# Optimization experiments

Hardware: AMD Instinct MI355X
Metric: run time of the kernel (lower is better)

Reference implementation:

```python
import jax, jax.numpy as jnp
import numpy as np

N_NODES = 100000   # n_nodes
N_EDGES = 1600000  # n_nodes * avg_degree(16)
D_IN = 128
D_OUT = 128


def setup_inputs() -> dict:
    key = jax.random.key(0)
    k1, k2, k3, k4, k5 = jax.random.split(key, 5)
    h = jax.random.normal(k1, (N_NODES, D_IN), dtype=jnp.float32)
    edge_src = jax.random.randint(k2, (N_EDGES,), 0, N_NODES, dtype=jnp.int32)
    edge_dst = jax.random.randint(k3, (N_EDGES,), 0, N_NODES, dtype=jnp.int32)
    # Linear params, init per reset_parameters: U(-stdv, stdv), stdv = 1/sqrt(in_feats)
    stdv = 1.0 / np.sqrt(D_IN)
    W = jax.random.uniform(k4, (D_OUT, D_IN), dtype=jnp.float32, minval=-stdv, maxval=stdv)
    b = jax.random.uniform(k5, (D_OUT,), dtype=jnp.float32, minval=-stdv, maxval=stdv)
    return {"h": h, "edge_src": edge_src, "edge_dst": edge_dst, "W": W, "b": b}


def reference(h, edge_src, edge_dst, W, b):
    # update_all(copy_src('h'), sum) == neighbor-sum aggregation (SpMM with 0/1 adjacency)
    ah = jax.ops.segment_sum(h[edge_src], edge_dst, num_segments=N_NODES)  # [N, D_IN]
    # dense linear + activation fused on the aggregated features
    return jax.nn.relu(ah @ W.T + b)  # [N, D_OUT]
```

## Files before the change

kernel.cpp:

```cpp
#include <hip/hip_runtime.h>

#define D 128
#define BKT_SHIFT 9
#define BKT_SIZE 512
#define P1_EPB 4096
#define CNT_EPB 8192
#define SW_LDU 68

typedef __attribute__((ext_vector_type(8))) short bf16x8;
typedef __attribute__((ext_vector_type(4))) float f32x4;

__device__ inline unsigned int pack2bf(float a, float b) {
    unsigned int ua = __float_as_uint(a);
    unsigned int ub = __float_as_uint(b);
    ua = (ua + 0x7fffu + ((ua >> 16) & 1u)) >> 16;
    ub = (ub + 0x7fffu + ((ub >> 16) & 1u)) >> 16;
    return ua | (ub << 16);
}
__device__ inline unsigned short pack1bf(float a) {
    unsigned int ua = __float_as_uint(a);
    return (unsigned short)((ua + 0x7fffu + ((ua >> 16) & 1u)) >> 16);
}


__global__ __launch_bounds__(256) void bucket_count_kernel(
    const int* __restrict__ edst, int* __restrict__ bucketCnt, int n_edges, int nbk)
{
    __shared__ int hcnt[256];
    const int tid = threadIdx.x;
    hcnt[tid] = 0;
    __syncthreads();
    const int base = blockIdx.x * CNT_EPB;
    const int lim = min(CNT_EPB, n_edges - base);
    for (int k = tid; k < lim; k += 256)
        atomicAdd(&hcnt[edst[base + k] >> BKT_SHIFT], 1);
    __syncthreads();
    if (tid < nbk && hcnt[tid] > 0) atomicAdd(&bucketCnt[tid], hcnt[tid]);
}

__global__ __launch_bounds__(256) void bucket_scan_kernel(
    const int* __restrict__ bucketCnt, int* __restrict__ bucketBase,
    int* __restrict__ bucketCur, int nbk)
{
    __shared__ int s[256];
    const int t = threadIdx.x;
    int v = (t < nbk) ? bucketCnt[t] : 0;
    s[t] = v;
    __syncthreads();
    #pragma unroll
    for (int off = 1; off < 256; off <<= 1) {
        int x = (t >= off) ? s[t - off] : 0;
        __syncthreads();
        s[t] += x;
        __syncthreads();
    }
    if (t < nbk) {
        int base = s[t] - v;
        bucketBase[t] = base;
        bucketCur[t] = base;
    }
}

__global__ __launch_bounds__(256) void p1_partition_kernel(
    const int* __restrict__ esrc, const int* __restrict__ edst,
    int* __restrict__ bucketCur, unsigned int* __restrict__ pairs, int n_edges)
{
    __shared__ int hcnt[256];
    __shared__ int hbase[256];
    const int tid = threadIdx.x;
    const int base = blockIdx.x * P1_EPB;
    hcnt[tid] = 0;
    __syncthreads();
    unsigned int pk[16]; int bk[16];
    #pragma unroll
    for (int k = 0; k < 16; k++) {
        int e = base + k * 256 + tid;
        if (e < n_edges) {
            int sv = esrc[e], dv = edst[e];
            bk[k] = dv >> BKT_SHIFT;
            pk[k] = ((unsigned)sv << BKT_SHIFT) | (unsigned)(dv & (BKT_SIZE - 1));
            atomicAdd(&hcnt[bk[k]], 1);
        } else bk[k] = -1;
    }
    __syncthreads();
    int cval = hcnt[tid];
    if (cval > 0) hbase[tid] = atomicAdd(&bucketCur[tid], cval);
    hcnt[tid] = 0;
    __syncthreads();
    #pragma unroll
    for (int k = 0; k < 16; k++) {
        if (bk[k] >= 0) {
            int loc = atomicAdd(&hcnt[bk[k]], 1);
            pairs[hbase[bk[k]] + loc] = pk[k];
        }
    }
}

__global__ __launch_bounds__(256) void p2_sort_kernel(
    const unsigned int* __restrict__ pairs, const int* __restrict__ bucketBase,
    int* __restrict__ sorted_src, int* __restrict__ gstart, int* __restrict__ gend,
    int n_nodes, int n_edges, int nbk)
{
    __shared__ int hist[BKT_SIZE];
    __shared__ int cur[BKT_SIZE];
    __shared__ int sb[256];
    const int tid = threadIdx.x;
    const int bkt = blockIdx.x;
    const int nbase = bkt << BKT_SHIFT;
    const int pstart = bucketBase[bkt];
    const int pend = (bkt == nbk - 1) ? n_edges : bucketBase[bkt + 1];
    hist[tid] = 0; hist[tid + 256] = 0;
    __syncthreads();
    for (int j = pstart + tid; j < pend; j += 256)
        atomicAdd(&hist[pairs[j] & (BKT_SIZE - 1)], 1);
    __syncthreads();
    int a  = hist[2 * tid];
    int b2 = hist[2 * tid + 1];
    int psum = a + b2;
    sb[tid] = psum;
    __syncthreads();
    #pragma unroll
    for (int off = 1; off < 256; off <<= 1) {
        int x = (tid >= off) ? sb[tid - off] : 0;
        __syncthreads();
        sb[tid] += x;
        __syncthreads();
    }
    int pexcl = sb[tid] - psum;
    cur[2 * tid] = pexcl;
    cur[2 * tid + 1] = pexcl + a;
    __syncthreads();
    for (int i = tid; i < BKT_SIZE; i += 256) {
        int nd = nbase + i;
        if (nd < n_nodes) {
            int st = pstart + cur[i];
            gstart[nd] = st;
            gend[nd] = st + hist[i];
        }
    }
    __syncthreads();
    for (int j = pstart + tid; j < pend; j += 256) {
        unsigned int p = pairs[j];
        int local = p & (BKT_SIZE - 1);
        int pos = pstart + atomicAdd(&cur[local], 1);
        sorted_src[pos] = (int)(p >> BKT_SHIFT);
    }
}

__global__ __launch_bounds__(256) void gemm_z_kernel(
    const float* __restrict__ h, const float* __restrict__ W,
    unsigned short* __restrict__ z, int n_nodes)
{
    __shared__ unsigned int sW[128 * SW_LDU];
    const int tid = threadIdx.x;
    for (int i = tid; i < 4096; i += 256) {
        float4 w = ((const float4*)W)[i];
        int row = i >> 5, c4 = i & 31;
        unsigned int* dst = &sW[row * SW_LDU + c4 * 2];
        dst[0] = pack2bf(w.x, w.y);
        dst[1] = pack2bf(w.z, w.w);
    }
    __syncthreads();

    const int wave = tid >> 6;
    const int lane = tid & 63;
    const int m = lane & 15;
    const int q = lane >> 4;
    const int r0 = blockIdx.x * 64 + wave * 16;
    const int arow = r0 + m;
    const bool rvalid = arow < n_nodes;

    bf16x8 afrag[4];
    #pragma unroll
    for (int ks = 0; ks < 4; ks++) {
        float4 x = make_float4(0.f, 0.f, 0.f, 0.f), y = x;
        if (rvalid) {
            const float4* p = (const float4*)(h + (size_t)arow * D + ks * 32 + q * 8);
            x = p[0]; y = p[1];
        }
        union { unsigned int u[4]; bf16x8 v; } cvt;
        cvt.u[0] = pack2bf(x.x, x.y);
        cvt.u[1] = pack2bf(x.z, x.w);
        cvt.u[2] = pack2bf(y.x, y.y);
        cvt.u[3] = pack2bf(y.z, y.w);
        afrag[ks] = cvt.v;
    }

    f32x4 acc[8];
    #pragma unroll
    for (int ct = 0; ct < 8; ct++) acc[ct] = (f32x4){0.f, 0.f, 0.f, 0.f};

    #pragma unroll
    for (int ct = 0; ct < 8; ct++) {
        #pragma unroll
        for (int ks = 0; ks < 4; ks++) {
            const unsigned int* p = &sW[(ct * 16 + m) * SW_LDU + ks * 16 + q * 4];
            union { uint4 u; bf16x8 v; } bu;
            bu.u = *(const uint4*)p;
            acc[ct] = __builtin_amdgcn_mfma_f32_16x16x32_bf16(afrag[ks], bu.v, acc[ct], 0, 0, 0);
        }
    }

    #pragma unroll
    for (int ct = 0; ct < 8; ct++) {
        int col = ct * 16 + m;
        #pragma unroll
        for (int i = 0; i < 4; i++) {
            int r = r0 + q * 4 + i;
            if (r < n_nodes) z[(size_t)r * D + col] = pack1bf(acc[ct][i]);
        }
    }
}

__global__ __launch_bounds__(256) void gather_row_kernel(
    const unsigned short* __restrict__ z, const int* __restrict__ gstart,
    const int* __restrict__ gend, const int* __restrict__ sorted_src,
    const float* __restrict__ b, float* __restrict__ out, int n_nodes)
{
    const int tid = threadIdx.x;
    const int node = blockIdx.x * 16 + (tid >> 4);
    const int lane = tid & 15;
    if (node >= n_nodes) return;
    int e = gstart[node];
    const int end = gend[node];
    const uint4* __restrict__ z4 = (const uint4*)z;
    float acc[8];
    #pragma unroll
    for (int i = 0; i < 8; i++) acc[i] = 0.f;
#define ADDV(v) do { \
    acc[0] += __uint_as_float((v).x << 16); acc[1] += __uint_as_float((v).x & 0xffff0000u); \
    acc[2] += __uint_as_float((v).y << 16); acc[3] += __uint_as_float((v).y & 0xffff0000u); \
    acc[4] += __uint_as_float((v).z << 16); acc[5] += __uint_as_float((v).z & 0xffff0000u); \
    acc[6] += __uint_as_float((v).w << 16); acc[7] += __uint_as_float((v).w & 0xffff0000u); } while (0)
    for (; e + 4 <= end; e += 4) {
        int s0 = sorted_src[e + 0];
        int s1 = sorted_src[e + 1];
        int s2 = sorted_src[e + 2];
        int s3 = sorted_src[e + 3];
        uint4 v0 = z4[(size_t)s0 * 16 + lane];
        uint4 v1 = z4[(size_t)s1 * 16 + lane];
        uint4 v2 = z4[(size_t)s2 * 16 + lane];
        uint4 v3 = z4[(size_t)s3 * 16 + lane];
        ADDV(v0); ADDV(v1); ADDV(v2); ADDV(v3);
    }
    for (; e < end; e++) {
        uint4 v = z4[(size_t)sorted_src[e] * 16 + lane];
        ADDV(v);
    }
#undef ADDV
    float4 b0 = ((const float4*)b)[lane * 2];
    float4 b1 = ((const float4*)b)[lane * 2 + 1];
    float4* o = (float4*)(out + (size_t)node * D + lane * 8);
    o[0] = make_float4(fmaxf(acc[0] + b0.x, 0.f), fmaxf(acc[1] + b0.y, 0.f),
                       fmaxf(acc[2] + b0.z, 0.f), fmaxf(acc[3] + b0.w, 0.f));
    o[1] = make_float4(fmaxf(acc[4] + b1.x, 0.f), fmaxf(acc[5] + b1.y, 0.f),
                       fmaxf(acc[6] + b1.z, 0.f), fmaxf(acc[7] + b1.w, 0.f));
}


__global__ __launch_bounds__(256) void hist_kernel(
    const int* __restrict__ edst, int* __restrict__ cnt, int n_edges)
{
    int gid = blockIdx.x * 256 + threadIdx.x;
    if (gid < n_edges) atomicAdd(&cnt[edst[gid]], 1);
}

__global__ __launch_bounds__(256) void scanA_kernel(
    const int* __restrict__ cnt, int* __restrict__ localoff,
    int* __restrict__ blocksums, int n)
{
    __shared__ int s[256];
    const int t = threadIdx.x;
    const int base = blockIdx.x * 1024 + t * 4;
    int v[4]; int sum = 0;
    #pragma unroll
    for (int i = 0; i < 4; i++) {
        int idx = base + i;
        v[i] = (idx < n) ? cnt[idx] : 0;
        sum += v[i];
    }
    s[t] = sum;
    __syncthreads();
    #pragma unroll
    for (int off = 1; off < 256; off <<= 1) {
        int x = (t >= off) ? s[t - off] : 0;
        __syncthreads();
        s[t] += x;
        __syncthreads();
    }
    int excl = s[t] - sum;
    int run = 0;
    #pragma unroll
    for (int i = 0; i < 4; i++) {
        int idx = base + i;
        if (idx < n) localoff[idx] = excl + run;
        run += v[i];
    }
    if (t == 255) blocksums[blockIdx.x] = s[255];
}

__global__ __launch_bounds__(256) void scanB_kernel(
    const int* __restrict__ blocksums, int* __restrict__ blockoffs, int nb)
{
    __shared__ int s[256];
    const int t = threadIdx.x;
    int v = (t < nb) ? blocksums[t] : 0;
    s[t] = v;
    __syncthreads();
    #pragma unroll
    for (int off = 1; off < 256; off <<= 1) {
        int x = (t >= off) ? s[t - off] : 0;
        __syncthreads();
        s[t] += x;
        __syncthreads();
    }
    if (t < nb) blockoffs[t] = s[t] - v;
}

__global__ __launch_bounds__(256) void scanC_kernel(
    const int* __restrict__ localoff, const int* __restrict__ blockoffs,
    int* __restrict__ outoffs, int* __restrict__ cursor, int n)
{
    int gid = blockIdx.x * 256 + threadIdx.x;
    if (gid >= n) return;
    int v = localoff[gid] + blockoffs[blockIdx.x >> 2];
    outoffs[gid] = v;
    if (cursor) cursor[gid] = v;
}

__global__ __launch_bounds__(256) void place_kernel(
    const int* __restrict__ esrc, const int* __restrict__ edst,
    int* __restrict__ cursor, int* __restrict__ sorted_src, int n_edges)
{
    int gid = blockIdx.x * 256 + threadIdx.x;
    if (gid >= n_edges) return;
    int d = edst[gid];
    int pos = atomicAdd(&cursor[d], 1);
    sorted_src[pos] = esrc[gid];
}

__global__ __launch_bounds__(256) void gather_kernel(
    const float* __restrict__ h, const int* __restrict__ offs,
    const int* __restrict__ endp, const int* __restrict__ sorted_src,
    float* __restrict__ out, int n_nodes)
{
    const int tid = threadIdx.x;
    const int node = blockIdx.x * 8 + (tid >> 5);
    const int lane = tid & 31;
    if (node >= n_nodes) return;
    const int start = offs[node];
    const int end = endp[node];
    const float4* __restrict__ h4 = (const float4*)h;
    float4 acc = make_float4(0.f, 0.f, 0.f, 0.f);
    for (int e = start; e < end; e++) {
        float4 a = h4[(size_t)sorted_src[e] * 32 + lane];
        acc.x += a.x; acc.y += a.y; acc.z += a.z; acc.w += a.w;
    }
    ((float4*)out)[(size_t)node * 32 + lane] = acc;
}

__global__ __launch_bounds__(256) void scatter_kernel(
    const float* __restrict__ h, const int* __restrict__ esrc,
    const int* __restrict__ edst, float* __restrict__ out, int n_edges)
{
    int gid = blockIdx.x * 256 + threadIdx.x;
    int e = gid >> 5;
    int l = gid & 31;
    if (e >= n_edges) return;
    int s = esrc[e];
    int d = edst[e];
    float4 v = ((const float4*)(h + (size_t)s * D))[l];
    float* o = out + (size_t)d * D + (size_t)l * 4;
    atomicAdd(o + 0, v.x);
    atomicAdd(o + 1, v.y);
    atomicAdd(o + 2, v.z);
    atomicAdd(o + 3, v.w);
}

__global__ __launch_bounds__(256) void mfma_gemm_relu_kernel(
    float* __restrict__ io, const float* __restrict__ W,
    const float* __restrict__ b, int n_nodes)
{
    __shared__ unsigned int sW[128 * SW_LDU];
    const int tid = threadIdx.x;
    for (int i = tid; i < 4096; i += 256) {
        float4 w = ((const float4*)W)[i];
        int row = i >> 5, c4 = i & 31;
        unsigned int* dst = &sW[row * SW_LDU + c4 * 2];
        dst[0] = pack2bf(w.x, w.y);
        dst[1] = pack2bf(w.z, w.w);
    }
    __syncthreads();
    const int wave = tid >> 6;
    const int lane = tid & 63;
    const int m = lane & 15;
    const int q = lane >> 4;
    const int r0 = blockIdx.x * 64 + wave * 16;
    const int arow = r0 + m;
    const bool rvalid = arow < n_nodes;
    bf16x8 afrag[4];
    #pragma unroll
    for (int ks = 0; ks < 4; ks++) {
        float4 x = make_float4(0.f, 0.f, 0.f, 0.f), y = x;
        if (rvalid) {
            const float4* p = (const float4*)(io + (size_t)arow * D + ks * 32 + q * 8);
            x = p[0]; y = p[1];
        }
        union { unsigned int u[4]; bf16x8 v; } cvt;
        cvt.u[0] = pack2bf(x.x, x.y);
        cvt.u[1] = pack2bf(x.z, x.w);
        cvt.u[2] = pack2bf(y.x, y.y);
        cvt.u[3] = pack2bf(y.z, y.w);
        afrag[ks] = cvt.v;
    }
    f32x4 acc[8];
    #pragma unroll
    for (int ct = 0; ct < 8; ct++) acc[ct] = (f32x4){0.f, 0.f, 0.f, 0.f};
    #pragma unroll
    for (int ct = 0; ct < 8; ct++) {
        #pragma unroll
        for (int ks = 0; ks < 4; ks++) {
            const unsigned int* p = &sW[(ct * 16 + m) * SW_LDU + ks * 16 + q * 4];
            union { uint4 u; bf16x8 v; } bu;
            bu.u = *(const uint4*)p;
            acc[ct] = __builtin_amdgcn_mfma_f32_16x16x32_bf16(afrag[ks], bu.v, acc[ct], 0, 0, 0);
        }
    }
    #pragma unroll
    for (int ct = 0; ct < 8; ct++) {
        int col = ct * 16 + m;
        float bias = b[col];
        #pragma unroll
        for (int i = 0; i < 4; i++) {
            int r = r0 + q * 4 + i;
            if (r < n_nodes) {
                float v = acc[ct][i] + bias;
                io[(size_t)r * D + col] = v > 0.f ? v : 0.f;
            }
        }
    }
}

extern "C" void kernel_launch(void* const* d_in, const int* in_sizes, int n_in,
                              void* d_out, int out_size, void* d_ws, size_t ws_size,
                              hipStream_t stream) {
    const float* h    = (const float*)d_in[0];
    const int*   esrc = (const int*)d_in[1];
    const int*   edst = (const int*)d_in[2];
    const float* W    = (const float*)d_in[3];
    const float* b    = (const float*)d_in[4];
    float* out = (float*)d_out;
    const int n_nodes = in_sizes[0] / D;
    const int n_edges = in_sizes[1];
    const int NB  = (n_nodes + 1023) / 1024;
    const int NBK = (n_nodes + BKT_SIZE - 1) / BKT_SIZE;

    size_t zone_bytes = (size_t)n_edges * 4;
    size_t zb2 = (size_t)n_nodes * D * 2;
    if (zb2 > zone_bytes) zone_bytes = zb2;
    size_t fixed = ((size_t)2 * n_nodes + 3 * NBK + (size_t)n_edges) * 4;
    size_t zone_off = (fixed + 15) & ~(size_t)15;
    size_t need_main = zone_off + zone_bytes;

    if (ws_size >= need_main && NBK <= 256 && n_nodes <= (1 << 23)) {
        int* gstart     = (int*)d_ws;
        int* gend       = gstart + n_nodes;
        int* bucketCnt  = gend + n_nodes;
        int* bucketBase = bucketCnt + NBK;
        int* bucketCur  = bucketBase + NBK;
        int* sorted_src = bucketCur + NBK;
        void* zone = (char*)d_ws + zone_off;
        unsigned int* pairs = (unsigned int*)zone;
        unsigned short* z = (unsigned short*)zone;

        hipMemsetAsync(bucketCnt, 0, (size_t)NBK * sizeof(int), stream);
        bucket_count_kernel<<<(n_edges + CNT_EPB - 1) / CNT_EPB, 256, 0, stream>>>(
            edst, bucketCnt, n_edges, NBK);
        bucket_scan_kernel<<<1, 256, 0, stream>>>(bucketCnt, bucketBase, bucketCur, NBK);
        p1_partition_kernel<<<(n_edges + P1_EPB - 1) / P1_EPB, 256, 0, stream>>>(
            esrc, edst, bucketCur, pairs, n_edges);
        p2_sort_kernel<<<NBK, 256, 0, stream>>>(
            pairs, bucketBase, sorted_src, gstart, gend, n_nodes, n_edges, NBK);
        gemm_z_kernel<<<(n_nodes + 63) / 64, 256, 0, stream>>>(h, W, z, n_nodes);
        gather_row_kernel<<<(n_nodes + 15) / 16, 256, 0, stream>>>(
            z, gstart, gend, sorted_src, b, out, n_nodes);
        return;
    }

    size_t csr_ints = (size_t)3 * n_nodes + 2 * NB + (size_t)n_edges;
    size_t needB = csr_ints * sizeof(int);
    if (ws_size >= needB && NB <= 256) {
        int* cnt        = (int*)d_ws;
        int* offs       = cnt + n_nodes;
        int* cursor     = offs + n_nodes;
        int* blocksums  = cursor + n_nodes;
        int* blockoffs  = blocksums + NB;
        int* sorted_src = blockoffs + NB;

        hipMemsetAsync(cnt, 0, (size_t)n_nodes * sizeof(int), stream);
        hist_kernel<<<(n_edges + 255) / 256, 256, 0, stream>>>(edst, cnt, n_edges);
        scanA_kernel<<<NB, 256, 0, stream>>>(cnt, offs, blocksums, n_nodes);
        scanB_kernel<<<1, 256, 0, stream>>>(blocksums, blockoffs, NB);
        scanC_kernel<<<(n_nodes + 255) / 256, 256, 0, stream>>>(
            offs, blockoffs, cnt, cursor, n_nodes);
        place_kernel<<<(n_edges + 255) / 256, 256, 0, stream>>>(
            esrc, edst, cursor, sorted_src, n_edges);
        gather_kernel<<<(n_nodes + 7) / 8, 256, 0, stream>>>(
            h, cnt, cursor, sorted_src, out, n_nodes);
    } else {
        hipMemsetAsync(out, 0, (size_t)n_nodes * D * sizeof(float), stream);
        long long total = (long long)n_edges * 32;
        scatter_kernel<<<(int)((total + 255) / 256), 256, 0, stream>>>(h, esrc, edst, out, n_edges);
    }
    mfma_gemm_relu_kernel<<<(n_nodes + 63) / 64, 256, 0, stream>>>(out, W, b, n_nodes);
}
```

Measured before the change: 261.9 us.

## Fuse CSR build and GEMM into one cooperative persistent kernel

Replaces the memset and the bucket count, scan, partition, sort and GEMM launches with a single cooperative kernel of 256 blocks. The phases are separated by grid.sync and share one union of shared-memory buffers, which removes the gaps between launches. The gather kernel now gives each node 32 lanes loading uint2 instead of 16 lanes loading uint4, and the old CSR fallback path is removed. The trade-off is that each phase runs with only one block per CU in a fixed grid, which may hide memory latency less well in the GEMM and partition phases, and grid-wide barriers add their own cost.

New measurement: 415.3 us. +58.6%, slower.

```diff
diff --git a/kernel.cpp b/kernel.cpp
--- a/kernel.cpp
+++ b/kernel.cpp
@@ -1,4 +1,7 @@
 #include <hip/hip_runtime.h>
+#include <hip/hip_cooperative_groups.h>
+
+namespace cg = cooperative_groups;
 
 #define D 128
 #define BKT_SHIFT 9
@@ -6,6 +9,7 @@
 #define P1_EPB 4096
 #define CNT_EPB 8192
 #define SW_LDU 68
+#define COOP_G 256
 
 typedef __attribute__((ext_vector_type(8))) short bf16x8;
 typedef __attribute__((ext_vector_type(4))) float f32x4;
@@ -20,6 +24,236 @@
 __device__ inline unsigned short pack1bf(float a) {
     unsigned int ua = __float_as_uint(a);
     return (unsigned short)((ua + 0x7fffu + ((ua >> 16) & 1u)) >> 16);
+}
+
+union SMem {
+    struct { int hcnt[256]; int hbase[256]; } c;
+    struct { int hist[BKT_SIZE]; int cur[BKT_SIZE]; int sb[256]; } d;
+    unsigned int sW[128 * SW_LDU];
+};
+
+__global__ __launch_bounds__(256) void build_all_kernel(
+    const float* __restrict__ h, const int* __restrict__ esrc,
+    const int* __restrict__ edst, const float* __restrict__ W,
+    int* __restrict__ gstart, int* __restrict__ gend,
+    int* __restrict__ bucketCnt, int* __restrict__ bucketBase,
+    int* __restrict__ bucketCur, int* __restrict__ sorted_src,
+    unsigned int* __restrict__ pairs, unsigned short* __restrict__ z,
+    int n_nodes, int n_edges, int nbk)
+{
+    __shared__ SMem sm;
+    cg::grid_group grid = cg::this_grid();
+    const int tid = threadIdx.x;
+    const int bid = blockIdx.x;
+    const int G = gridDim.x;
+
+    if (bid == 0 && tid < nbk) bucketCnt[tid] = 0;
+    sm.c.hcnt[tid] = 0;
+    __syncthreads();
+    for (int e = bid * 256 + tid; e < n_edges; e += G * 256)
+        atomicAdd(&sm.c.hcnt[edst[e] >> BKT_SHIFT], 1);
+    __syncthreads();
+    grid.sync();
+    if (tid < nbk && sm.c.hcnt[tid] > 0) atomicAdd(&bucketCnt[tid], sm.c.hcnt[tid]);
+    grid.sync();
+
+    if (bid == 0) {
+        int v = (tid < nbk) ? bucketCnt[tid] : 0;
+        sm.d.sb[tid] = v;
+        __syncthreads();
+        #pragma unroll
+        for (int off = 1; off < 256; off <<= 1) {
+            int x = (tid >= off) ? sm.d.sb[tid - off] : 0;
+            __syncthreads();
+            sm.d.sb[tid] += x;
+            __syncthreads();
+        }
+        if (tid < nbk) {
+            int base = sm.d.sb[tid] - v;
+            bucketBase[tid] = base;
+            bucketCur[tid] = base;
+        }
+    }
+    grid.sync();
+
+    const int nchunks = (n_edges + P1_EPB - 1) / P1_EPB;
+    for (int chunk = bid; chunk < nchunks; chunk += G) {
+        const int base = chunk * P1_EPB;
+        sm.c.hcnt[tid] = 0;
+        __syncthreads();
+        unsigned int pk[16]; int bk[16];
+        #pragma unroll
+        for (int k = 0; k < 16; k++) {
+            int e = base + k * 256 + tid;
+            if (e < n_edges) {
+                int sv = esrc[e], dv = edst[e];
+                bk[k] = dv >> BKT_SHIFT;
+                pk[k] = ((unsigned)sv << BKT_SHIFT) | (unsigned)(dv & (BKT_SIZE - 1));
+                atomicAdd(&sm.c.hcnt[bk[k]], 1);
+            } else bk[k] = -1;
+        }
+        __syncthreads();
+        int cval = sm.c.hcnt[tid];
+        if (cval > 0) sm.c.hbase[tid] = atomicAdd(&bucketCur[tid], cval);
+        __syncthreads();
+        sm.c.hcnt[tid] = 0;
+        __syncthreads();
+        #pragma unroll
+        for (int k = 0; k < 16; k++) {
+            if (bk[k] >= 0) {
+                int loc = atomicAdd(&sm.c.hcnt[bk[k]], 1);
+                pairs[sm.c.hbase[bk[k]] + loc] = pk[k];
+            }
+        }
+        __syncthreads();
+    }
+    grid.sync();
+
+    for (int bkt = bid; bkt < nbk; bkt += G) {
+        const int nbase = bkt << BKT_SHIFT;
+        const int pstart = bucketBase[bkt];
+        const int pend = (bkt == nbk - 1) ? n_edges : bucketBase[bkt + 1];
+        sm.d.hist[tid] = 0; sm.d.hist[tid + 256] = 0;
+        __syncthreads();
+        for (int j = pstart + tid; j < pend; j += 256)
+            atomicAdd(&sm.d.hist[pairs[j] & (BKT_SIZE - 1)], 1);
+        __syncthreads();
+        int a  = sm.d.hist[2 * tid];
+        int b2 = sm.d.hist[2 * tid + 1];
+        int psum = a + b2;
+        sm.d.sb[tid] = psum;
+        __syncthreads();
+        #pragma unroll
+        for (int off = 1; off < 256; off <<= 1) {
+            int x = (tid >= off) ? sm.d.sb[tid - off] : 0;
+            __syncthreads();
+            sm.d.sb[tid] += x;
+            __syncthreads();
+        }
+        int pexcl = sm.d.sb[tid] - psum;
+        sm.d.cur[2 * tid] = pexcl;
+        sm.d.cur[2 * tid + 1] = pexcl + a;
+        __syncthreads();
+        for (int i = tid; i < BKT_SIZE; i += 256) {
+            int nd = nbase + i;
+            if (nd < n_nodes) {
+                int st = pstart + sm.d.cur[i];
+                gstart[nd] = st;
+                gend[nd] = st + sm.d.hist[i];
+            }
+        }
+        __syncthreads();
+        for (int j = pstart + tid; j < pend; j += 256) {
+            unsigned int p = pairs[j];
+            int local = p & (BKT_SIZE - 1);
+            int pos = pstart + atomicAdd(&sm.d.cur[local], 1);
+            sorted_src[pos] = (int)(p >> BKT_SHIFT);
+        }
+        __syncthreads();
+    }
+    grid.sync();
+
+    for (int i = tid; i < 4096; i += 256) {
+        float4 w = ((const float4*)W)[i];
+        int row = i >> 5, c4 = i & 31;
+        unsigned int* dst = &sm.sW[row * SW_LDU + c4 * 2];
+        dst[0] = pack2bf(w.x, w.y);
+        dst[1] = pack2bf(w.z, w.w);
+    }
+    __syncthreads();
+    const int wave = tid >> 6;
+    const int lane = tid & 63;
+    const int m = lane & 15;
+    const int q = lane >> 4;
+    const int ntiles = (n_nodes + 63) / 64;
+    for (int tile = bid; tile < ntiles; tile += G) {
+        const int r0 = tile * 64 + wave * 16;
+        const int arow = r0 + m;
+        const bool rvalid = arow < n_nodes;
+        bf16x8 afrag[4];
+        #pragma unroll
+        for (int ks = 0; ks < 4; ks++) {
+            float4 x = make_float4(0.f, 0.f, 0.f, 0.f), y = x;
+            if (rvalid) {
+                const float4* p = (const float4*)(h + (size_t)arow * D + ks * 32 + q * 8);
+                x = p[0]; y = p[1];
+            }
+            union { unsigned int u[4]; bf16x8 v; } cvt;
+            cvt.u[0] = pack2bf(x.x, x.y);
+            cvt.u[1] = pack2bf(x.z, x.w);
+            cvt.u[2] = pack2bf(y.x, y.y);
+            cvt.u[3] = pack2bf(y.z, y.w);
+            afrag[ks] = cvt.v;
+        }
+        f32x4 acc[8];
+        #pragma unroll
+        for (int ct = 0; ct < 8; ct++) acc[ct] = (f32x4){0.f, 0.f, 0.f, 0.f};
+        #pragma unroll
+        for (int ct = 0; ct < 8; ct++) {
+            #pragma unroll
+            for (int ks = 0; ks < 4; ks++) {
+                const unsigned int* p = &sm.sW[(ct * 16 + m) * SW_LDU + ks * 16 + q * 4];
+                union { uint4 u; bf16x8 v; } bu;
+                bu.u = *(const uint4*)p;
+                acc[ct] = __builtin_amdgcn_mfma_f32_16x16x32_bf16(afrag[ks], bu.v, acc[ct], 0, 0, 0);
+            }
+        }
+        #pragma unroll
+        for (int ct = 0; ct < 8; ct++) {
+            int col = ct * 16 + m;
+            #pragma unroll
+            for (int i = 0; i < 4; i++) {
+                int r = r0 + q * 4 + i;
+                if (r < n_nodes) z[(size_t)r * D + col] = pack1bf(acc[ct][i]);
+            }
+        }
+    }
+}
+
+__global__ __launch_bounds__(256) void gather_row_kernel(
+    const unsigned short* __restrict__ z, const int* __restrict__ gstart,
+    const int* __restrict__ gend, const int* __restrict__ sorted_src,
+    const float* __restrict__ b, float* __restrict__ out, int n_nodes)
+{
+    const int tid = threadIdx.x;
+    const int node = blockIdx.x * 8 + (tid >> 5);
+    const int lane = tid & 31;
+    if (node >= n_nodes) return;
+    int e = gstart[node];
+    const int end = gend[node];
+    const uint2* __restrict__ z2 = (const uint2*)z;
+    float4 acc = make_float4(0.f, 0.f, 0.f, 0.f);
+    for (; e + 4 <= end; e += 4) {
+        int s0 = sorted_src[e + 0];
+        int s1 = sorted_src[e + 1];
+        int s2 = sorted_src[e + 2];
+        int s3 = sorted_src[e + 3];
+        uint2 v0 = z2[(size_t)s0 * 32 + lane];
+        uint2 v1 = z2[(size_t)s1 * 32 + lane];
+        uint2 v2 = z2[(size_t)s2 * 32 + lane];
+        uint2 v3 = z2[(size_t)s3 * 32 + lane];
+        acc.x += __uint_as_float(v0.x << 16) + __uint_as_float(v1.x << 16)
+               + __uint_as_float(v2.x << 16) + __uint_as_float(v3.x << 16);
+        acc.y += __uint_as_float(v0.x & 0xffff0000u) + __uint_as_float(v1.x & 0xffff0000u)
+               + __uint_as_float(v2.x & 0xffff0000u) + __uint_as_float(v3.x & 0xffff0000u);
+        acc.z += __uint_as_float(v0.y << 16) + __uint_as_float(v1.y << 16)
+               + __uint_as_float(v2.y << 16) + __uint_as_float(v3.y << 16);
+        acc.w += __uint_as_float(v0.y & 0xffff0000u) + __uint_as_float(v1.y & 0xffff0000u)
+               + __uint_as_float(v2.y & 0xffff0000u) + __uint_as_float(v3.y & 0xffff0000u);
+    }
+    for (; e < end; e++) {
+        uint2 v = z2[(size_t)sorted_src[e] * 32 + lane];
+        acc.x += __uint_as_float(v.x << 16);
+        acc.y += __uint_as_float(v.x & 0xffff0000u);
+        acc.z += __uint_as_float(v.y << 16);
+        acc.w += __uint_as_float(v.y & 0xffff0000u);
+    }
+    float4 bb = ((const float4*)b)[lane];
+    float vx = acc.x + bb.x, vy = acc.y + bb.y;
+    float vz = acc.z + bb.z, vw = acc.w + bb.w;
+    ((float4*)out)[(size_t)node * 32 + lane] = make_float4(
+        vx > 0.f ? vx : 0.f, vy > 0.f ? vy : 0.f,
+        vz > 0.f ? vz : 0.f, vw > 0.f ? vw : 0.f);
 }
 
 
@@ -85,6 +319,7 @@
     __syncthreads();
     int cval = hcnt[tid];
     if (cval > 0) hbase[tid] = atomicAdd(&bucketCur[tid], cval);
+    __syncthreads();
     hcnt[tid] = 0;
     __syncthreads();
     #pragma unroll
@@ -161,7 +396,6 @@
         dst[1] = pack2bf(w.z, w.w);
     }
     __syncthreads();
-
     const int wave = tid >> 6;
     const int lane = tid & 63;
     const int m = lane & 15;
@@ -169,7 +403,6 @@
     const int r0 = blockIdx.x * 64 + wave * 16;
     const int arow = r0 + m;
     const bool rvalid = arow < n_nodes;
-
     bf16x8 afrag[4];
     #pragma unroll
     for (int ks = 0; ks < 4; ks++) {
@@ -185,11 +418,9 @@
         cvt.u[3] = pack2bf(y.z, y.w);
         afrag[ks] = cvt.v;
     }
-
     f32x4 acc[8];
     #pragma unroll
     for (int ct = 0; ct < 8; ct++) acc[ct] = (f32x4){0.f, 0.f, 0.f, 0.f};
-
     #pragma unroll
     for (int ct = 0; ct < 8; ct++) {
         #pragma unroll
@@ -200,7 +431,6 @@
             acc[ct] = __builtin_amdgcn_mfma_f32_16x16x32_bf16(afrag[ks], bu.v, acc[ct], 0, 0, 0);
         }
     }
-
     #pragma unroll
     for (int ct = 0; ct < 8; ct++) {
         int col = ct * 16 + m;
@@ -212,152 +442,6 @@
     }
 }
 
-__global__ __launch_bounds__(256) void gather_row_kernel(
-    const unsigned short* __restrict__ z, const int* __restrict__ gstart,
-    const int* __restrict__ gend, const int* __restrict__ sorted_src,
-    const float* __restrict__ b, float* __restrict__ out, int n_nodes)
-{
-    const int tid = threadIdx.x;
-    const int node = blockIdx.x * 16 + (tid >> 4);
-    const int lane = tid & 15;
-    if (node >= n_nodes) return;
-    int e = gstart[node];
-    const int end = gend[node];
-    const uint4* __restrict__ z4 = (const uint4*)z;
-    float acc[8];
-    #pragma unroll
-    for (int i = 0; i < 8; i++) acc[i] = 0.f;
-#define ADDV(v) do { \
-    acc[0] += __uint_as_float((v).x << 16); acc[1] += __uint_as_float((v).x & 0xffff0000u); \
-    acc[2] += __uint_as_float((v).y << 16); acc[3] += __uint_as_float((v).y & 0xffff0000u); \
-    acc[4] += __uint_as_float((v).z << 16); acc[5] += __uint_as_float((v).z & 0xffff0000u); \
-    acc[6] += __uint_as_float((v).w << 16); acc[7] += __uint_as_float((v).w & 0xffff0000u); } while (0)
-    for (; e + 4 <= end; e += 4) {
-        int s0 = sorted_src[e + 0];
-        int s1 = sorted_src[e + 1];
-        int s2 = sorted_src[e + 2];
-        int s3 = sorted_src[e + 3];
-        uint4 v0 = z4[(size_t)s0 * 16 + lane];
-        uint4 v1 = z4[(size_t)s1 * 16 + lane];
-        uint4 v2 = z4[(size_t)s2 * 16 + lane];
-        uint4 v3 = z4[(size_t)s3 * 16 + lane];
-        ADDV(v0); ADDV(v1); ADDV(v2); ADDV(v3);
-    }
-    for (; e < end; e++) {
-        uint4 v = z4[(size_t)sorted_src[e] * 16 + lane];
-        ADDV(v);
-    }
-#undef ADDV
-    float4 b0 = ((const float4*)b)[lane * 2];
-    float4 b1 = ((const float4*)b)[lane * 2 + 1];
-    float4* o = (float4*)(out + (size_t)node * D + lane * 8);
-    o[0] = make_float4(fmaxf(acc[0] + b0.x, 0.f), fmaxf(acc[1] + b0.y, 0.f),
-                       fmaxf(acc[2] + b0.z, 0.f), fmaxf(acc[3] + b0.w, 0.f));
-    o[1] = make_float4(fmaxf(acc[4] + b1.x, 0.f), fmaxf(acc[5] + b1.y, 0.f),
-                       fmaxf(acc[6] + b1.z, 0.f), fmaxf(acc[7] + b1.w, 0.f));
-}
-
-
-__global__ __launch_bounds__(256) void hist_kernel(
-    const int* __restrict__ edst, int* __restrict__ cnt, int n_edges)
-{
-    int gid = blockIdx.x * 256 + threadIdx.x;
-    if (gid < n_edges) atomicAdd(&cnt[edst[gid]], 1);
-}
-
-__global__ __launch_bounds__(256) void scanA_kernel(
-    const int* __restrict__ cnt, int* __restrict__ localoff,
-    int* __restrict__ blocksums, int n)
-{
-    __shared__ int s[256];
-    const int t = threadIdx.x;
-    const int base = blockIdx.x * 1024 + t * 4;
-    int v[4]; int sum = 0;
-    #pragma unroll
-    for (int i = 0; i < 4; i++) {
-        int idx = base + i;
-        v[i] = (idx < n) ? cnt[idx] : 0;
-        sum += v[i];
-    }
-    s[t] = sum;
-    __syncthreads();
-    #pragma unroll
-    for (int off = 1; off < 256; off <<= 1) {
-        int x = (t >= off) ? s[t - off] : 0;
-        __syncthreads();
-        s[t] += x;
-        __syncthreads();
-    }
-    int excl = s[t] - sum;
-    int run = 0;
-    #pragma unroll
-    for (int i = 0; i < 4; i++) {
-        int idx = base + i;
-        if (idx < n) localoff[idx] = excl + run;
-        run += v[i];
-    }
-    if (t == 255) blocksums[blockIdx.x] = s[255];
-}
-
-__global__ __launch_bounds__(256) void scanB_kernel(
-    const int* __restrict__ blocksums, int* __restrict__ blockoffs, int nb)
-{
-    __shared__ int s[256];
-    const int t = threadIdx.x;
-    int v = (t < nb) ? blocksums[t] : 0;
-    s[t] = v;
-    __syncthreads();
-    #pragma unroll
-    for (int off = 1; off < 256; off <<= 1) {
-        int x = (t >= off) ? s[t - off] : 0;
-        __syncthreads();
-        s[t] += x;
-        __syncthreads();
-    }
-    if (t < nb) blockoffs[t] = s[t] - v;
-}
-
-__global__ __launch_bounds__(256) void scanC_kernel(
-    const int* __restrict__ localoff, const int* __restrict__ blockoffs,
-    int* __restrict__ outoffs, int* __restrict__ cursor, int n)
-{
-    int gid = blockIdx.x * 256 + threadIdx.x;
-    if (gid >= n) return;
-    int v = localoff[gid] + blockoffs[blockIdx.x >> 2];
-    outoffs[gid] = v;
-    if (cursor) cursor[gid] = v;
-}
-
-__global__ __launch_bounds__(256) void place_kernel(
-    const int* __restrict__ esrc, const int* __restrict__ edst,
-    int* __restrict__ cursor, int* __restrict__ sorted_src, int n_edges)
-{
-    int gid = blockIdx.x * 256 + threadIdx.x;
-    if (gid >= n_edges) return;
-    int d = edst[gid];
-    int pos = atomicAdd(&cursor[d], 1);
-    sorted_src[pos] = esrc[gid];
-}
-
-__global__ __launch_bounds__(256) void gather_kernel(
-    const float* __restrict__ h, const int* __restrict__ offs,
-    const int* __restrict__ endp, const int* __restrict__ sorted_src,
-    float* __restrict__ out, int n_nodes)
-{
-    const int tid = threadIdx.x;
-    const int node = blockIdx.x * 8 + (tid >> 5);
-    const int lane = tid & 31;
-    if (node >= n_nodes) return;
-    const int start = offs[node];
-    const int end = endp[node];
-    const float4* __restrict__ h4 = (const float4*)h;
-    float4 acc = make_float4(0.f, 0.f, 0.f, 0.f);
-    for (int e = start; e < end; e++) {
-        float4 a = h4[(size_t)sorted_src[e] * 32 + lane];
-        acc.x += a.x; acc.y += a.y; acc.z += a.z; acc.w += a.w;
-    }
-    ((float4*)out)[(size_t)node * 32 + lane] = acc;
-}
 
 __global__ __launch_bounds__(256) void scatter_kernel(
     const float* __restrict__ h, const int* __restrict__ esrc,
@@ -452,7 +536,6 @@
     float* out = (float*)d_out;
     const int n_nodes = in_sizes[0] / D;
     const int n_edges = in_sizes[1];
-    const int NB  = (n_nodes + 1023) / 1024;
     const int NBK = (n_nodes + BKT_SIZE - 1) / BKT_SIZE;
 
     size_t zone_bytes = (size_t)n_edges * 4;
@@ -473,44 +556,33 @@
         unsigned int* pairs = (unsigned int*)zone;
         unsigned short* z = (unsigned short*)zone;
 
-        hipMemsetAsync(bucketCnt, 0, (size_t)NBK * sizeof(int), stream);
-        bucket_count_kernel<<<(n_edges + CNT_EPB - 1) / CNT_EPB, 256, 0, stream>>>(
-            edst, bucketCnt, n_edges, NBK);
-        bucket_scan_kernel<<<1, 256, 0, stream>>>(bucketCnt, bucketBase, bucketCur, NBK);
-        p1_partition_kernel<<<(n_edges + P1_EPB - 1) / P1_EPB, 256, 0, stream>>>(
-            esrc, edst, bucketCur, pairs, n_edges);
-        p2_sort_kernel<<<NBK, 256, 0, stream>>>(
-            pairs, bucketBase, sorted_src, gstart, gend, n_nodes, n_edges, NBK);
-        gemm_z_kernel<<<(n_nodes + 63) / 64, 256, 0, stream>>>(h, W, z, n_nodes);
-        gather_row_kernel<<<(n_nodes + 15) / 16, 256, 0, stream>>>(
+        void* kargs[] = {
+            (void*)&h, (void*)&esrc, (void*)&edst, (void*)&W,
+            (void*)&gstart, (void*)&gend,
+            (void*)&bucketCnt, (void*)&bucketBase, (void*)&bucketCur,
+            (void*)&sorted_src, (void*)&pairs, (void*)&z,
+            (void*)&n_nodes, (void*)&n_edges, (void*)&NBK
+        };
+        hipError_t cerr = hipLaunchCooperativeKernel(
+            (void*)build_all_kernel, dim3(COOP_G), dim3(256), kargs, 0, stream);
+        if (cerr != hipSuccess) {
+            hipMemsetAsync(bucketCnt, 0, (size_t)NBK * sizeof(int), stream);
+            bucket_count_kernel<<<(n_edges + CNT_EPB - 1) / CNT_EPB, 256, 0, stream>>>(
+                edst, bucketCnt, n_edges, NBK);
+            bucket_scan_kernel<<<1, 256, 0, stream>>>(bucketCnt, bucketBase, bucketCur, NBK);
+            p1_partition_kernel<<<(n_edges + P1_EPB - 1) / P1_EPB, 256, 0, stream>>>(
+                esrc, edst, bucketCur, pairs, n_edges);
+            p2_sort_kernel<<<NBK, 256, 0, stream>>>(
+                pairs, bucketBase, sorted_src, gstart, gend, n_nodes, n_edges, NBK);
+            gemm_z_kernel<<<(n_nodes + 63) / 64, 256, 0, stream>>>(h, W, z, n_nodes);
+        }
+        gather_row_kernel<<<(n_nodes + 7) / 8, 256, 0, stream>>>(
             z, gstart, gend, sorted_src, b, out, n_nodes);
         return;
     }
 
-    size_t csr_ints = (size_t)3 * n_nodes + 2 * NB + (size_t)n_edges;
-    size_t needB = csr_ints * sizeof(int);
-    if (ws_size >= needB && NB <= 256) {
-        int* cnt        = (int*)d_ws;
-        int* offs       = cnt + n_nodes;
-        int* cursor     = offs + n_nodes;
-        int* blocksums  = cursor + n_nodes;
-        int* blockoffs  = blocksums + NB;
-        int* sorted_src = blockoffs + NB;
-
-        hipMemsetAsync(cnt, 0, (size_t)n_nodes * sizeof(int), stream);
-        hist_kernel<<<(n_edges + 255) / 256, 256, 0, stream>>>(edst, cnt, n_edges);
-        scanA_kernel<<<NB, 256, 0, stream>>>(cnt, offs, blocksums, n_nodes);
-        scanB_kernel<<<1, 256, 0, stream>>>(blocksums, blockoffs, NB);
-        scanC_kernel<<<(n_nodes + 255) / 256, 256, 0, stream>>>(
-            offs, blockoffs, cnt, cursor, n_nodes);
-        place_kernel<<<(n_edges + 255) / 256, 256, 0, stream>>>(
-            esrc, edst, cursor, sorted_src, n_edges);
-        gather_kernel<<<(n_nodes + 7) / 8, 256, 0, stream>>>(
-            h, cnt, cursor, sorted_src, out, n_nodes);
-    } else {
-        hipMemsetAsync(out, 0, (size_t)n_nodes * D * sizeof(float), stream);
-        long long total = (long long)n_edges * 32;
-        scatter_kernel<<<(int)((total + 255) / 256), 256, 0, stream>>>(h, esrc, edst, out, n_edges);
-    }
+    hipMemsetAsync(out, 0, (size_t)n_nodes * D * sizeof(float), stream);
+    long long total = (long long)n_edges * 32;
+    scatter_kernel<<<(int)((total + 255) / 256), 256, 0, stream>>>(h, esrc, edst, out, n_edges);
     mfma_gemm_relu_kernel<<<(n_nodes + 63) / 64, 256, 0, stream>>>(out, W, b, n_nodes);
 }
```
